# Kernel optimization log

Hardware: AMD Instinct MI355X
Metric: run time of the kernel (lower is better)

The kernel has to match this reference:

```python
import jax, jax.numpy as jnp
import numpy as np

N, E, F, H = 50000, 800000, 64, 4
NEG_SLOPE = 0.2
LN_EPS = 1e-5


def setup_inputs() -> dict:
    key = jax.random.key(0)
    ks = jax.random.split(key, 12)
    h = jax.random.normal(ks[0], (N, F), dtype=jnp.float32)
    src = jax.random.randint(ks[1], (E,), 0, N, dtype=jnp.int32)
    dst = jax.random.randint(ks[2], (E,), 0, N, dtype=jnp.int32)
    s = 1.0 / np.sqrt(F)
    fc_w = jax.random.uniform(ks[3], (F, H * F), jnp.float32, -s, s)
    attn_l = jax.random.normal(ks[4], (H, F), dtype=jnp.float32) * s
    attn_r = jax.random.normal(ks[5], (H, F), dtype=jnp.float32) * s
    gat_bias = jnp.zeros((H * F,), dtype=jnp.float32)
    so = 1.0 / np.sqrt(H * F)
    out_w = jax.random.uniform(ks[6], (H * F, F), jnp.float32, -so, so)
    out_b = jax.random.uniform(ks[7], (F,), jnp.float32, -so, so)
    ln_g = jnp.ones((F,), dtype=jnp.float32)
    ln_b = jnp.zeros((F,), dtype=jnp.float32)
    return {"h": h, "src": src, "dst": dst, "fc_w": fc_w, "attn_l": attn_l,
            "attn_r": attn_r, "gat_bias": gat_bias, "out_w": out_w,
            "out_b": out_b, "ln_g": ln_g, "ln_b": ln_b}


def reference(h, src, dst, fc_w, attn_l, attn_r, gat_bias, out_w, out_b, ln_g, ln_b):
    # --- GATConv (DGL semantics) ---
    feat = (h @ fc_w).reshape(N, H, F)                      # [N,H,F]
    el = jnp.einsum('nhf,hf->nh', feat, attn_l)             # [N,H]
    er = jnp.einsum('nhf,hf->nh', feat, attn_r)             # [N,H]
    e = jax.nn.leaky_relu(el[src] + er[dst], NEG_SLOPE)     # [E,H]
    # edge softmax over incoming edges of each dst node
    m = jax.ops.segment_max(e, dst, num_segments=N)         # [N,H]
    ex = jnp.exp(e - m[dst])                                # [E,H]
    z = jax.ops.segment_sum(ex, dst, num_segments=N)        # [N,H]
    alpha = ex / z[dst]                                     # [E,H]
    msg = feat[src] * alpha[:, :, None]                     # [E,H,F]
    rst = jax.ops.segment_sum(msg, dst, num_segments=N)     # [N,H,F]
    rst = rst + gat_bias.reshape(H, F)
    # --- out linear + layernorm ---
    x = rst.reshape(N, H * F) @ out_w + out_b               # [N,F]
    mu = jnp.mean(x, axis=-1, keepdims=True)
    var = jnp.var(x, axis=-1, keepdims=True)
    return (x - mu) * jax.lax.rsqrt(var + LN_EPS) * ln_g + ln_b
```

## Files before the change

### kernel.cpp

```cpp
#include <hip/hip_runtime.h>

#define NN 50000
#define EE 800000
#define FF 64
#define HH 4
#define HF 256
#define NEG_SLOPE 0.2f
#define LN_EPS 1e-5f
#define WPACK_N (4 * 8 * 64 * 8)
#define WPACKA_N (16 * 2 * 64 * 8)
#define NTILE (NN / 16)

typedef __attribute__((ext_vector_type(8))) short s8v;
typedef __attribute__((ext_vector_type(4))) float f4v;

__device__ __forceinline__ unsigned short f32_to_bf16_rne(float x) {
  unsigned int u = __float_as_uint(x);
  unsigned int r = u + 0x7FFFu + ((u >> 16) & 1u);
  return (unsigned short)(r >> 16);
}

__device__ __forceinline__ float readlane_f(float v, int l) {
  return __uint_as_float(
      (unsigned)__builtin_amdgcn_readlane((int)__float_as_uint(v), l));
}

__global__ __launch_bounds__(256) void k_prep(
    const float* __restrict__ fc_w, const float* __restrict__ out_w,
    unsigned short* __restrict__ wpackA, unsigned short* __restrict__ wpack,
    int* __restrict__ cnt) {
  const int idx = blockIdx.x * 256 + threadIdx.x;
  if (idx < WPACKA_N) {
    const int j = idx & 7;
    const int l = (idx >> 3) & 63;
    const int t = (idx >> 9) & 1;
    const int ct = idx >> 10;
    const int k = 32 * t + (l >> 4) * 8 + j;
    const int c = 16 * ct + (l & 15);
    wpackA[idx] = f32_to_bf16_rne(fc_w[k * HF + c]);
  } else if (idx < WPACKA_N + WPACK_N) {
    const int i2 = idx - WPACKA_N;
    const int j = i2 & 7;
    const int l = (i2 >> 3) & 63;
    const int t = (i2 >> 9) & 7;
    const int ct = i2 >> 12;
    const int k = 32 * t + (l >> 4) * 8 + j;
    const int c = 16 * ct + (l & 15);
    wpack[i2] = f32_to_bf16_rne(out_w[k * FF + c]);
  }
  if (idx < NN) cnt[idx] = 0;
}

__global__ __launch_bounds__(256) void k_feat(
    const float* __restrict__ h, const unsigned short* __restrict__ wpackA,
    const float* __restrict__ attn_l, const float* __restrict__ attn_r,
    unsigned short* __restrict__ featb, float* __restrict__ el,
    float* __restrict__ er) {
  __shared__ unsigned short wlds[WPACKA_N];
  {
    const uint4* s = (const uint4*)wpackA;
    uint4* d = (uint4*)wlds;
    for (int i = threadIdx.x; i < 2048; i += 256) d[i] = s[i];
  }
  __syncthreads();
  const int wave = threadIdx.x >> 6;
  const int lane = threadIdx.x & 63;
  const int tile = blockIdx.x * 4 + wave;
  if (tile >= NTILE) return;
  const int n0 = tile * 16;
  const int cl = lane & 15;
  const int quad = lane >> 4;

  float al[16], ar[16];
#pragma unroll
  for (int ct = 0; ct < 16; ++ct) {
    al[ct] = attn_l[16 * ct + cl];
    ar[ct] = attn_r[16 * ct + cl];
  }

  s8v a[2];
#pragma unroll
  for (int t = 0; t < 2; ++t) {
    const float* hp = h + (size_t)(n0 + cl) * FF + 32 * t + quad * 8;
    float hv[8];
    *(float4*)hv = *(const float4*)hp;
    *(float4*)(hv + 4) = *(const float4*)(hp + 4);
    s8v av;
#pragma unroll
    for (int i = 0; i < 8; ++i) av[i] = (short)f32_to_bf16_rne(hv[i]);
    a[t] = av;
  }

  f4v acc[16];
#pragma unroll
  for (int ct = 0; ct < 16; ++ct) {
    f4v z = {0.f, 0.f, 0.f, 0.f};
    acc[ct] = z;
#pragma unroll
    for (int t = 0; t < 2; ++t) {
      const s8v b = *(const s8v*)(wlds + ((ct * 2 + t) * 64 + lane) * 8);
      acc[ct] = __builtin_amdgcn_mfma_f32_16x16x32_bf16(a[t], b, acc[ct], 0, 0, 0);
    }
  }

#pragma unroll
  for (int r = 0; r < 4; ++r) {
    const int n = n0 + quad * 4 + r;
    float pl[4] = {0.f, 0.f, 0.f, 0.f};
    float pr[4] = {0.f, 0.f, 0.f, 0.f};
#pragma unroll
    for (int g = 0; g < 4; ++g) {
      const float x0 = acc[g][r];
      const float x1 = acc[g + 4][r];
      const float x2 = acc[g + 8][r];
      const float x3 = acc[g + 12][r];
      uint2 pk;
      pk.x = (unsigned)f32_to_bf16_rne(x0) | ((unsigned)f32_to_bf16_rne(x1) << 16);
      pk.y = (unsigned)f32_to_bf16_rne(x2) | ((unsigned)f32_to_bf16_rne(x3) << 16);
      *(uint2*)(featb + (size_t)n * HF + (16 * g + cl) * 4) = pk;
      pl[0] = fmaf(x0, al[g], pl[0]);      pr[0] = fmaf(x0, ar[g], pr[0]);
      pl[1] = fmaf(x1, al[g + 4], pl[1]);  pr[1] = fmaf(x1, ar[g + 4], pr[1]);
      pl[2] = fmaf(x2, al[g + 8], pl[2]);  pr[2] = fmaf(x2, ar[g + 8], pr[2]);
      pl[3] = fmaf(x3, al[g + 12], pl[3]); pr[3] = fmaf(x3, ar[g + 12], pr[3]);
    }
#pragma unroll
    for (int off = 1; off < 16; off <<= 1) {
#pragma unroll
      for (int hh = 0; hh < 4; ++hh) {
        pl[hh] += __shfl_xor(pl[hh], off, 64);
        pr[hh] += __shfl_xor(pr[hh], off, 64);
      }
    }
    if (cl == 0) {
      *(float4*)(el + (size_t)n * 4) = make_float4(pl[0], pl[1], pl[2], pl[3]);
      *(float4*)(er + (size_t)n * 4) = make_float4(pr[0], pr[1], pr[2], pr[3]);
    }
  }
}

__global__ void k_scatter(const int* __restrict__ src,
                          const int* __restrict__ dst,
                          int* __restrict__ cnt, int* __restrict__ colp) {
  int e = blockIdx.x * blockDim.x + threadIdx.x;
  if (e < EE) {
    const int d = dst[e];
    const int pos = atomicAdd(&cnt[d], 1);
    if (pos < 64) colp[(d << 6) | pos] = src[e];
  }
}

__global__ __launch_bounds__(256) void k_gather(
    const unsigned short* __restrict__ featb, const float* __restrict__ el,
    const float* __restrict__ er, const int* __restrict__ cnt,
    const int* __restrict__ colp, const float* __restrict__ gat_bias,
    unsigned short* __restrict__ rstb) {
  const int wave = threadIdx.x >> 6;
  const int lane = threadIdx.x & 63;
  const int gw = blockIdx.x * 4 + wave;
  const int stride = gridDim.x * 4;
  const float gb0 = gat_bias[lane], gb1 = gat_bias[64 + lane];
  const float gb2 = gat_bias[128 + lane], gb3 = gat_bias[192 + lane];
  const unsigned short* fb = featb + lane * HH;
  for (int n = gw; n < NN; n += stride) {
    const int m = cnt[n];
    const float4 erv = *(const float4*)(er + (size_t)n * 4);
    float a0 = 0.f, a1 = 0.f, a2 = 0.f, a3 = 0.f;
    float z0 = 0.f, z1 = 0.f, z2 = 0.f, z3 = 0.f;
    float w0 = 0.f, w1 = 0.f, w2 = 0.f, w3 = 0.f;
    int s = 0;
    if (lane < m) {
      s = colp[(n << 6) | lane];
      const float4 elv = *(const float4*)(el + (size_t)s * 4);
      float e0 = elv.x + erv.x, e1 = elv.y + erv.y;
      float e2 = elv.z + erv.z, e3 = elv.w + erv.w;
      e0 = e0 > 0.f ? e0 : NEG_SLOPE * e0;
      e1 = e1 > 0.f ? e1 : NEG_SLOPE * e1;
      e2 = e2 > 0.f ? e2 : NEG_SLOPE * e2;
      e3 = e3 > 0.f ? e3 : NEG_SLOPE * e3;
      w0 = __expf(e0); w1 = __expf(e1);
      w2 = __expf(e2); w3 = __expf(e3);
    }
    for (int e = 0; e < m; e += 8) {
#pragma unroll
      for (int j = 0; j < 8; ++j) {
        const int le = e + j;
        const int se = __builtin_amdgcn_readlane(s, le);
        const float we0 = readlane_f(w0, le);
        const float we1 = readlane_f(w1, le);
        const float we2 = readlane_f(w2, le);
        const float we3 = readlane_f(w3, le);
        const uint2 d = *(const uint2*)(fb + (size_t)se * HF);
        z0 += we0; z1 += we1; z2 += we2; z3 += we3;
        a0 = fmaf(we0, __uint_as_float(d.x << 16), a0);
        a1 = fmaf(we1, __uint_as_float(d.x & 0xFFFF0000u), a1);
        a2 = fmaf(we2, __uint_as_float(d.y << 16), a2);
        a3 = fmaf(we3, __uint_as_float(d.y & 0xFFFF0000u), a3);
      }
    }
    unsigned short* rp = rstb + (size_t)n * HF + lane;
    rp[0]   = f32_to_bf16_rne((z0 > 0.f ? a0 / z0 : 0.f) + gb0);
    rp[64]  = f32_to_bf16_rne((z1 > 0.f ? a1 / z1 : 0.f) + gb1);
    rp[128] = f32_to_bf16_rne((z2 > 0.f ? a2 / z2 : 0.f) + gb2);
    rp[192] = f32_to_bf16_rne((z3 > 0.f ? a3 / z3 : 0.f) + gb3);
  }
}

__global__ __launch_bounds__(256) void k_out(
    const unsigned short* __restrict__ rstb,
    const unsigned short* __restrict__ wpack,
    const float* __restrict__ out_b, const float* __restrict__ ln_g,
    const float* __restrict__ ln_b, float* __restrict__ out) {
  __shared__ unsigned short wlds[WPACK_N];
  {
    const uint4* src = (const uint4*)wpack;
    uint4* dstp = (uint4*)wlds;
    for (int i = threadIdx.x; i < 2048; i += 256) dstp[i] = src[i];
  }
  __syncthreads();
  const int wave = threadIdx.x >> 6;
  const int lane = threadIdx.x & 63;
  const int tile = blockIdx.x * 4 + wave;
  if (tile >= NTILE) return;
  const int n0 = tile * 16;
  const int cl = lane & 15;
  const int quad = lane >> 4;

  const unsigned short* arow = rstb + (size_t)(n0 + cl) * HF + quad * 8;
  s8v a[8];
#pragma unroll
  for (int t = 0; t < 8; ++t) a[t] = *(const s8v*)(arow + 32 * t);

  f4v acc[4];
#pragma unroll
  for (int ct = 0; ct < 4; ++ct) {
    f4v z = {0.f, 0.f, 0.f, 0.f};
    acc[ct] = z;
#pragma unroll
    for (int t = 0; t < 8; ++t) {
      const s8v b = *(const s8v*)(wlds + ((ct * 8 + t) * 64 + lane) * 8);
      acc[ct] = __builtin_amdgcn_mfma_f32_16x16x32_bf16(a[t], b, acc[ct], 0, 0, 0);
    }
  }

  float x[4][4];
  float s1[4], s2[4];
#pragma unroll
  for (int r = 0; r < 4; ++r) { s1[r] = 0.f; s2[r] = 0.f; }
#pragma unroll
  for (int ct = 0; ct < 4; ++ct) {
    const float ob = out_b[16 * ct + cl];
#pragma unroll
    for (int r = 0; r < 4; ++r) {
      const float v = acc[ct][r] + ob;
      x[ct][r] = v;
      s1[r] += v;
      s2[r] += v * v;
    }
  }
#pragma unroll
  for (int r = 0; r < 4; ++r) {
#pragma unroll
    for (int off = 1; off < 16; off <<= 1) {
      s1[r] += __shfl_xor(s1[r], off, 64);
      s2[r] += __shfl_xor(s2[r], off, 64);
    }
  }
#pragma unroll
  for (int r = 0; r < 4; ++r) {
    const float mu = s1[r] * (1.f / 64.f);
    const float var = s2[r] * (1.f / 64.f) - mu * mu;
    const float inv = rsqrtf(var + LN_EPS);
    const int row = n0 + quad * 4 + r;
#pragma unroll
    for (int ct = 0; ct < 4; ++ct) {
      const int c = 16 * ct + cl;
      out[(size_t)row * FF + c] = (x[ct][r] - mu) * inv * ln_g[c] + ln_b[c];
    }
  }
}

extern "C" void kernel_launch(void* const* d_in, const int* in_sizes, int n_in,
                              void* d_out, int out_size, void* d_ws,
                              size_t ws_size, hipStream_t stream) {
  const float* h_in   = (const float*)d_in[0];
  const int*   src    = (const int*)d_in[1];
  const int*   dst    = (const int*)d_in[2];
  const float* fc_w   = (const float*)d_in[3];
  const float* attn_l = (const float*)d_in[4];
  const float* attn_r = (const float*)d_in[5];
  const float* gbias  = (const float*)d_in[6];
  const float* out_w  = (const float*)d_in[7];
  const float* out_b  = (const float*)d_in[8];
  const float* ln_g   = (const float*)d_in[9];
  const float* ln_b   = (const float*)d_in[10];
  float* out = (float*)d_out;

  char* p = (char*)d_ws;
  auto alloc = [&](size_t bytes) {
    char* q = p;
    p += (bytes + 255) & ~(size_t)255;
    return q;
  };
  unsigned short* featb  = (unsigned short*)alloc((size_t)NN * HF * 2);
  unsigned short* rstb   = (unsigned short*)alloc((size_t)NN * HF * 2);
  unsigned short* wpack  = (unsigned short*)alloc((size_t)WPACK_N * 2);
  unsigned short* wpackA = (unsigned short*)alloc((size_t)WPACKA_N * 2);
  float* el      = (float*)alloc((size_t)NN * HH * 4);
  float* er      = (float*)alloc((size_t)NN * HH * 4);
  int*   cnt     = (int*)alloc((size_t)NN * 4);
  int*   colp    = (int*)alloc((size_t)NN * 64 * 4);

  k_prep<<<256, 256, 0, stream>>>(fc_w, out_w, wpackA, wpack, cnt);
  k_feat<<<(NTILE + 3) / 4, 256, 0, stream>>>(h_in, wpackA, attn_l, attn_r,
                                              featb, el, er);
  k_scatter<<<(EE + 255) / 256, 256, 0, stream>>>(src, dst, cnt, colp);
  k_gather<<<2048, 256, 0, stream>>>(featb, el, er, cnt, colp, gbias, rstb);
  k_out<<<(NTILE + 3) / 4, 256, 0, stream>>>(rstb, wpack, out_b, ln_g, ln_b, out);
}
```

Baseline: 217.6 us.

## Fuse edge gather with output projection and layernorm via LDS tile

Merges the gather/aggregate kernel with the output linear + layernorm kernel. Each block aggregates 16 destination nodes into an LDS tile, then one wave runs the MFMA projection and layernorm directly from that tile. This removes the bf16 rst round trip through global memory and one kernel launch. In exchange, three of four waves idle during the matmul phase, and B weights are read from global/cache instead of LDS.

After: 210.2 us. 1.04x faster.

```diff
diff --git a/kernel.cpp b/kernel.cpp
--- a/kernel.cpp
+++ b/kernel.cpp
@@ -10,6 +10,7 @@
 #define WPACK_N (4 * 8 * 64 * 8)
 #define WPACKA_N (16 * 2 * 64 * 8)
 #define NTILE (NN / 16)
+#define TROW 264
 
 typedef __attribute__((ext_vector_type(8))) short s8v;
 typedef __attribute__((ext_vector_type(4))) float f4v;
@@ -149,19 +150,25 @@
   }
 }
 
-__global__ __launch_bounds__(256) void k_gather(
+__global__ __launch_bounds__(256) void k_gather_out(
     const unsigned short* __restrict__ featb, const float* __restrict__ el,
     const float* __restrict__ er, const int* __restrict__ cnt,
     const int* __restrict__ colp, const float* __restrict__ gat_bias,
-    unsigned short* __restrict__ rstb) {
+    const unsigned short* __restrict__ wpack, const float* __restrict__ out_b,
+    const float* __restrict__ ln_g, const float* __restrict__ ln_b,
+    float* __restrict__ out) {
+  __shared__ unsigned short tile[16][TROW];
   const int wave = threadIdx.x >> 6;
   const int lane = threadIdx.x & 63;
-  const int gw = blockIdx.x * 4 + wave;
-  const int stride = gridDim.x * 4;
+  const int n0 = blockIdx.x * 16;
   const float gb0 = gat_bias[lane], gb1 = gat_bias[64 + lane];
   const float gb2 = gat_bias[128 + lane], gb3 = gat_bias[192 + lane];
   const unsigned short* fb = featb + lane * HH;
-  for (int n = gw; n < NN; n += stride) {
+
+#pragma unroll
+  for (int r = 0; r < 4; ++r) {
+    const int row = wave * 4 + r;
+    const int n = n0 + row;
     const int m = cnt[n];
     const float4 erv = *(const float4*)(er + (size_t)n * 4);
     float a0 = 0.f, a1 = 0.f, a2 = 0.f, a3 = 0.f;
@@ -197,38 +204,20 @@
         a3 = fmaf(we3, __uint_as_float(d.y & 0xFFFF0000u), a3);
       }
     }
-    unsigned short* rp = rstb + (size_t)n * HF + lane;
-    rp[0]   = f32_to_bf16_rne((z0 > 0.f ? a0 / z0 : 0.f) + gb0);
-    rp[64]  = f32_to_bf16_rne((z1 > 0.f ? a1 / z1 : 0.f) + gb1);
-    rp[128] = f32_to_bf16_rne((z2 > 0.f ? a2 / z2 : 0.f) + gb2);
-    rp[192] = f32_to_bf16_rne((z3 > 0.f ? a3 / z3 : 0.f) + gb3);
-  }
-}
-
-__global__ __launch_bounds__(256) void k_out(
-    const unsigned short* __restrict__ rstb,
-    const unsigned short* __restrict__ wpack,
-    const float* __restrict__ out_b, const float* __restrict__ ln_g,
-    const float* __restrict__ ln_b, float* __restrict__ out) {
-  __shared__ unsigned short wlds[WPACK_N];
-  {
-    const uint4* src = (const uint4*)wpack;
-    uint4* dstp = (uint4*)wlds;
-    for (int i = threadIdx.x; i < 2048; i += 256) dstp[i] = src[i];
+    tile[row][lane]       = f32_to_bf16_rne((z0 > 0.f ? a0 / z0 : 0.f) + gb0);
+    tile[row][64 + lane]  = f32_to_bf16_rne((z1 > 0.f ? a1 / z1 : 0.f) + gb1);
+    tile[row][128 + lane] = f32_to_bf16_rne((z2 > 0.f ? a2 / z2 : 0.f) + gb2);
+    tile[row][192 + lane] = f32_to_bf16_rne((z3 > 0.f ? a3 / z3 : 0.f) + gb3);
   }
   __syncthreads();
-  const int wave = threadIdx.x >> 6;
-  const int lane = threadIdx.x & 63;
-  const int tile = blockIdx.x * 4 + wave;
-  if (tile >= NTILE) return;
-  const int n0 = tile * 16;
+  if (wave != 0) return;
+
   const int cl = lane & 15;
   const int quad = lane >> 4;
-
-  const unsigned short* arow = rstb + (size_t)(n0 + cl) * HF + quad * 8;
   s8v a[8];
 #pragma unroll
-  for (int t = 0; t < 8; ++t) a[t] = *(const s8v*)(arow + 32 * t);
+  for (int t = 0; t < 8; ++t)
+    a[t] = *(const s8v*)(&tile[cl][32 * t + quad * 8]);
 
   f4v acc[4];
 #pragma unroll
@@ -237,7 +226,7 @@
     acc[ct] = z;
 #pragma unroll
     for (int t = 0; t < 8; ++t) {
-      const s8v b = *(const s8v*)(wlds + ((ct * 8 + t) * 64 + lane) * 8);
+      const s8v b = *(const s8v*)(wpack + ((ct * 8 + t) * 64 + lane) * 8);
       acc[ct] = __builtin_amdgcn_mfma_f32_16x16x32_bf16(a[t], b, acc[ct], 0, 0, 0);
     }
   }
@@ -302,7 +291,6 @@
     return q;
   };
   unsigned short* featb  = (unsigned short*)alloc((size_t)NN * HF * 2);
-  unsigned short* rstb   = (unsigned short*)alloc((size_t)NN * HF * 2);
   unsigned short* wpack  = (unsigned short*)alloc((size_t)WPACK_N * 2);
   unsigned short* wpackA = (unsigned short*)alloc((size_t)WPACKA_N * 2);
   float* el      = (float*)alloc((size_t)NN * HH * 4);
@@ -314,6 +302,6 @@
   k_feat<<<(NTILE + 3) / 4, 256, 0, stream>>>(h_in, wpackA, attn_l, attn_r,
                                               featb, el, er);
   k_scatter<<<(EE + 255) / 256, 256, 0, stream>>>(src, dst, cnt, colp);
-  k_gather<<<2048, 256, 0, stream>>>(featb, el, er, cnt, colp, gbias, rstb);
-  k_out<<<(NTILE + 3) / 4, 256, 0, stream>>>(rstb, wpack, out_b, ln_g, ln_b, out);
-}
+  k_gather_out<<<NTILE, 256, 0, stream>>>(featb, el, er, cnt, colp, gbias,
+                                          wpack, out_b, ln_g, ln_b, out);
+}
```
